# Performance work log

Hardware: AMD Instinct MI355X
Metric: run time of the kernel (lower is better)

Reference implementation:

```python
import jax, jax.numpy as jnp
import numpy as np

B, V, T, CIN, WEMB, H, NW = 32, 500, 24, 2, 4, 64, 8
C0 = CIN + WEMB  # 6 channels entering first layer


def _stglstm(x, supports, Wg, bg, Wo, bo, out_len=None, final_layer=False):
    # x: (B, C, V, T); supports: (S, V, V)
    Bb, C, Vv, Tt = x.shape
    T_steps = out_len if out_len is not None else Tt
    if final_layer:
        xs = jnp.broadcast_to(x[:, :, :, -1][None], (T_steps, Bb, C, Vv))
    else:
        xs = jnp.moveaxis(x, 3, 0)  # (T, B, C, V)

    def step(carry, xt):
        hx, cx = carry
        comb = xt + hx  # (B, C, V)
        feats = [comb]
        for s in range(supports.shape[0]):  # fixed small support_len loop
            x1 = jnp.einsum('bcv,vw->bcw', comb, supports[s])
            x2 = jnp.einsum('bcv,vw->bcw', x1, supports[s])
            feats += [x1, x2]  # order-2 diffusion
        g = jnp.concatenate(feats, axis=1)  # (B, 7C, V)
        gates = jnp.einsum('bgv,og->bov', g, Wg) + bg[None, :, None]  # (B, 4C, V)
        i, f, cg, o = jnp.split(gates, 4, axis=1)
        cy = jax.nn.sigmoid(f) * cx + jax.nn.sigmoid(i) * cg  # cellgate is linear (no tanh), as in source
        hy = jax.nn.sigmoid(o) * jnp.tanh(cy)
        return (hy, cy), hy

    h0 = jnp.zeros((Bb, C, Vv), x.dtype)
    _, hs = jax.lax.scan(step, (h0, h0), xs)  # hs: (T, B, C, V)
    hs = jnp.moveaxis(hs, 0, 3)  # (B, C, V, T)
    return jnp.einsum('bcvt,oc->bovt', hs, Wo) + bo[None, :, None, None]


def _se(x, Wa, Wb):
    y = x.mean(axis=(2, 3))  # (B, C) global avg pool
    y = jax.nn.sigmoid(jax.nn.relu(y @ Wa.T) @ Wb.T)
    return x * y[:, :, None, None]


def setup_inputs():
    key = jax.random.key(0)
    ks = jax.random.split(key, 24)

    def n(k, shape, s=0.05):
        return jax.random.normal(k, shape, jnp.float32) * s

    A = jax.random.uniform(ks[0], (3, V, V), jnp.float32)
    A = A / A.sum(-1, keepdims=True)  # row-stochastic random-walk matrices
    return {
        'x': n(ks[1], (B, CIN, V, T), 1.0),
        'supports': A,
        'w_type': jax.random.randint(ks[2], (B, V, T), 0, NW, dtype=jnp.int32),
        'Wemb': n(ks[3], (NW, WEMB)),
        'Wg0': n(ks[4], (4 * C0, 7 * C0)), 'bg0': jnp.zeros((4 * C0,), jnp.float32),
        'Wo0': n(ks[5], (H, C0)), 'bo0': jnp.zeros((H,), jnp.float32),
        'Ws0a': n(ks[6], (H // 16, H)), 'Ws0b': n(ks[7], (H, H // 16)),
        'Wg1': n(ks[8], (4 * H, 7 * H)), 'bg1': jnp.zeros((4 * H,), jnp.float32),
        'Wo1': n(ks[9], (H, H)), 'bo1': jnp.zeros((H,), jnp.float32),
        'Ws1a': n(ks[10], (H // 16, H)), 'Ws1b': n(ks[11], (H, H // 16)),
        'Wg2': n(ks[12], (4 * H, 7 * H)), 'bg2': jnp.zeros((4 * H,), jnp.float32),
        'Wo2': n(ks[13], (H, H)), 'bo2': jnp.zeros((H,), jnp.float32),
        'Wg3': n(ks[14], (4 * H, 7 * H)), 'bg3': jnp.zeros((4 * H,), jnp.float32),
        'Wo3': n(ks[15], (2, H)), 'bo3': jnp.zeros((2,), jnp.float32),
    }


def reference(x, supports, w_type, Wemb, Wg0, bg0, Wo0, bo0, Ws0a, Ws0b,
              Wg1, bg1, Wo1, bo1, Ws1a, Ws1b, Wg2, bg2, Wo2, bo2,
              Wg3, bg3, Wo3, bo3):
    w_vec = Wemb[w_type]  # (B, V, T, wemb)
    w_vec = jnp.transpose(w_vec, (0, 3, 1, 2))  # (B, wemb, V, T)
    h = jnp.concatenate([x, w_vec], axis=1)  # (B, CIN+wemb, V, T)
    h = _stglstm(h, supports, Wg0, bg0, Wo0, bo0)
    h = _se(h, Ws0a, Ws0b)
    h = _stglstm(h, supports, Wg1, bg1, Wo1, bo1)
    h = _se(h, Ws1a, Ws1b)
    h = _stglstm(h, supports, Wg2, bg2, Wo2, bo2)
    out = _stglstm(h, supports, Wg3, bg3, Wo3, bo3, out_len=T, final_layer=True)
    return out  # (B, 2, V, out_len)
```

## Files before the change

### kernel.cpp

```cpp
#include <hip/hip_runtime.h>
#include <math.h>

#define NV 500
#define NB 32
#define NT 24
#define NH 64

typedef _Float16 f16;
typedef _Float16 f16x8 __attribute__((ext_vector_type(8)));
typedef _Float16 f16x4 __attribute__((ext_vector_type(4)));
typedef float    f32x4 __attribute__((ext_vector_type(4)));

__device__ __forceinline__ float sigm(float x){ return 1.f/(1.f+expf(-x)); }

__global__ void k_a2(const float* __restrict__ A, float* __restrict__ A2)
{
    int idx = blockIdx.x*256 + threadIdx.x;
    if (idx >= 3*500*500) return;
    int wv = idx % 500; int rest = idx/500; int r = rest % 500; int s = rest/500;
    const float* Ar = A + ((size_t)s*500 + r)*500;
    const float* Ac = A + (size_t)s*500*500 + wv;
    float a = 0.f;
    for (int u = 0; u < 500; u++) a += Ar[u]*Ac[(size_t)u*500];
    A2[idx] = a;
}

__global__ void k_acat(const float* __restrict__ A, const float* __restrict__ A2,
                       f16* __restrict__ AcatT)
{
    int idx = blockIdx.x*256 + threadIdx.x;
    if (idx >= 3072*512) return;
    int k = idx & 511;
    int n = idx >> 9;
    int j = n >> 9, wv = n & 511;
    float val = 0.f;
    if (k < 500 && wv < 500) {
        int s = j >> 1;
        const float* M = (j & 1) ? A2 : A;
        val = M[((size_t)s*500 + k)*500 + wv];
    }
    AcatT[idx] = (f16)val;
}

__global__ void k_f2h(const float* __restrict__ src, f16* __restrict__ dst, int n)
{
    int idx = blockIdx.x*256 + threadIdx.x;
    if (idx < n) dst[idx] = (f16)src[idx];
}

__global__ __launch_bounds__(256)
void k_diff(const f16* __restrict__ Acv, const f16* __restrict__ Bt,
            f16* __restrict__ fout, int Mtot, int C, int G)
{
    __shared__ f16 lA[128*32];
    __shared__ f16 lB[128*32];
    const int tid = threadIdx.x;
    const int n0 = blockIdx.x*128, m0 = blockIdx.y*128;
    const int r0 = tid>>2, c0 = tid&3;
    const int swz0 = r0*32 + ((c0 ^ ((r0>>1)&3))<<3);
    const int swz1 = swz0 + 64*32;
    int mA0 = m0 + r0;      if (mA0 > Mtot-1) mA0 = Mtot-1;
    int mA1 = m0 + r0 + 64; if (mA1 > Mtot-1) mA1 = Mtot-1;
    const f16* gA0 = Acv + (size_t)mA0*512 + c0*8;
    const f16* gA1 = Acv + (size_t)mA1*512 + c0*8;
    const f16* gB0 = Bt + (size_t)(n0+r0)*512 + c0*8;
    const f16* gB1 = Bt + (size_t)(n0+r0+64)*512 + c0*8;

    const int w = tid>>6, lane = tid&63;
    const int wr = (w>>1)<<6, wc = (w&1)<<6;
    const int fm = lane&15, fk = lane>>4;
    const int fch = (fk ^ ((fm>>1)&3))<<3;

    f32x4 acc[4][4];
    #pragma unroll
    for (int i=0;i<4;i++)
        #pragma unroll
        for (int j=0;j<4;j++) acc[i][j] = (f32x4){0.f,0.f,0.f,0.f};

    f32x4 ra0 = *(const f32x4*)gA0, ra1 = *(const f32x4*)gA1;
    f32x4 rb0 = *(const f32x4*)gB0, rb1 = *(const f32x4*)gB1;

    for (int ks = 0; ks < 16; ks++) {
        __syncthreads();
        *(f32x4*)(lA + swz0) = ra0;  *(f32x4*)(lA + swz1) = ra1;
        *(f32x4*)(lB + swz0) = rb0;  *(f32x4*)(lB + swz1) = rb1;
        if (ks < 15) {
            int o = (ks+1)*32;
            ra0 = *(const f32x4*)(gA0 + o); ra1 = *(const f32x4*)(gA1 + o);
            rb0 = *(const f32x4*)(gB0 + o); rb1 = *(const f32x4*)(gB1 + o);
        }
        __syncthreads();
        f16x8 af[4], bf[4];
        #pragma unroll
        for (int i=0;i<4;i++) af[i] = *(const f16x8*)(lA + (wr + i*16 + fm)*32 + fch);
        #pragma unroll
        for (int j=0;j<4;j++) bf[j] = *(const f16x8*)(lB + (wc + j*16 + fm)*32 + fch);
        #pragma unroll
        for (int i=0;i<4;i++)
            #pragma unroll
            for (int j=0;j<4;j++)
                acc[i][j] = __builtin_amdgcn_mfma_f32_16x16x32_f16(af[i], bf[j], acc[i][j], 0, 0, 0);
    }

    #pragma unroll
    for (int j=0;j<4;j++) {
        int col = n0 + wc + j*16 + fm;
        int jb = col >> 9, wv = col & 511;
        if (wv >= 500) continue;
        #pragma unroll
        for (int i=0;i<4;i++) {
            int mb = m0 + wr + i*16 + fk*4;
            if (C == 64) {
                if (mb >= Mtot) continue;
                int b = mb >> 6, c = mb & 63;
                f16x4 h4;
                h4[0]=(f16)acc[i][j][0]; h4[1]=(f16)acc[i][j][1];
                h4[2]=(f16)acc[i][j][2]; h4[3]=(f16)acc[i][j][3];
                *(f16x4*)(fout + ((size_t)b*512 + wv)*G + C + jb*C + c) = h4;
            } else {
                #pragma unroll
                for (int r=0;r<4;r++) {
                    int m = mb + r;
                    if (m < Mtot) {
                        int b = m / C, c = m - b*C;
                        fout[((size_t)b*512 + wv)*G + C + jb*C + c] = (f16)acc[i][j][r];
                    }
                }
            }
        }
    }
}

__global__ __launch_bounds__(256)
void k_gates(const f16* __restrict__ fT, const f16* __restrict__ Wg,
             const float* __restrict__ bg, float* __restrict__ gT)
{
    __shared__ f16 lA[128*32];
    __shared__ f16 lB[128*32];
    const int tid = threadIdx.x;
    const int n0 = blockIdx.x*128, m0 = blockIdx.y*128, b = blockIdx.z;
    const f16* Ab = fT + (size_t)b*512*448;
    const int r0 = tid>>2, c0 = tid&3;
    const int swz0 = r0*32 + ((c0 ^ ((r0>>1)&3))<<3);
    const int swz1 = swz0 + 64*32;
    const f16* gA0 = Ab + (size_t)(m0+r0)*448 + c0*8;
    const f16* gA1 = Ab + (size_t)(m0+r0+64)*448 + c0*8;
    const f16* gB0 = Wg + (size_t)(n0+r0)*448 + c0*8;
    const f16* gB1 = Wg + (size_t)(n0+r0+64)*448 + c0*8;

    const int w = tid>>6, lane = tid&63;
    const int wr = (w>>1)<<6, wc = (w&1)<<6;
    const int fm = lane&15, fk = lane>>4;
    const int fch = (fk ^ ((fm>>1)&3))<<3;

    f32x4 acc[4][4];
    #pragma unroll
    for (int i=0;i<4;i++)
        #pragma unroll
        for (int j=0;j<4;j++) acc[i][j] = (f32x4){0.f,0.f,0.f,0.f};

    f32x4 ra0 = *(const f32x4*)gA0, ra1 = *(const f32x4*)gA1;
    f32x4 rb0 = *(const f32x4*)gB0, rb1 = *(const f32x4*)gB1;

    for (int ks = 0; ks < 14; ks++) {
        __syncthreads();
        *(f32x4*)(lA + swz0) = ra0;  *(f32x4*)(lA + swz1) = ra1;
        *(f32x4*)(lB + swz0) = rb0;  *(f32x4*)(lB + swz1) = rb1;
        if (ks < 13) {
            int o = (ks+1)*32;
            ra0 = *(const f32x4*)(gA0 + o); ra1 = *(const f32x4*)(gA1 + o);
            rb0 = *(const f32x4*)(gB0 + o); rb1 = *(const f32x4*)(gB1 + o);
        }
        __syncthreads();
        f16x8 af[4], bf[4];
        #pragma unroll
        for (int i=0;i<4;i++) af[i] = *(const f16x8*)(lA + (wr + i*16 + fm)*32 + fch);
        #pragma unroll
        for (int j=0;j<4;j++) bf[j] = *(const f16x8*)(lB + (wc + j*16 + fm)*32 + fch);
        #pragma unroll
        for (int i=0;i<4;i++)
            #pragma unroll
            for (int j=0;j<4;j++)
                acc[i][j] = __builtin_amdgcn_mfma_f32_16x16x32_f16(af[i], bf[j], acc[i][j], 0, 0, 0);
    }

    #pragma unroll
    for (int j=0;j<4;j++) {
        int o = n0 + wc + j*16 + fm;
        float bias = bg[o];
        #pragma unroll
        for (int i=0;i<4;i++) {
            int vb = m0 + wr + i*16 + fk*4;
            #pragma unroll
            for (int r=0;r<4;r++) {
                int v = vb + r;
                if (v < 500)
                    gT[((size_t)b*512 + v)*256 + o] = acc[i][j][r] + bias;
            }
        }
    }
}

__global__ __launch_bounds__(256)
void k_comb(const void* __restrict__ src, int srcF16, int Cin,
            const float* __restrict__ Wo, const float* __restrict__ bo,
            const float* __restrict__ se, const f16* __restrict__ hprev,
            f16* __restrict__ fT, f16* __restrict__ ccv)
{
    __shared__ float WoS[64*64];
    __shared__ float seS[64], boS[64];
    __shared__ f16 combS[64*72];
    int b = blockIdx.y, v0 = blockIdx.x*64;
    int tid = threadIdx.x;
    if (Cin > 0) {
        for (int i = tid; i < 64*Cin; i += 256) WoS[i] = Wo[i];
        if (tid < 64) { boS[tid] = bo[tid]; seS[tid] = se ? se[b*64+tid] : 1.f; }
    }
    __syncthreads();
    int vloc = tid>>2, part = tid&3;
    int v = v0 + vloc;
    float val[16];
    if (Cin == 0) {
        const float* x3 = (const float*)src + ((size_t)b*512 + v)*64 + part*16;
        #pragma unroll
        for (int k=0;k<16;k++) val[k] = x3[k];
    } else {
        float acc[16];
        #pragma unroll
        for (int k=0;k<16;k++) acc[k] = 0.f;
        if (srcF16) {
            const f16* sp = (const f16*)src + ((size_t)b*512 + v)*64;
            for (int cc=0; cc<Cin; cc++) {
                float xv = (float)sp[cc];
                #pragma unroll
                for (int k=0;k<16;k++) acc[k] += WoS[(part*16+k)*Cin + cc]*xv;
            }
        } else {
            const float* sp = (const float*)src + ((size_t)b*512 + v)*(size_t)Cin;
            for (int cc=0; cc<Cin; cc++) {
                float xv = sp[cc];
                #pragma unroll
                for (int k=0;k<16;k++) acc[k] += WoS[(part*16+k)*Cin + cc]*xv;
            }
        }
        #pragma unroll
        for (int k=0;k<16;k++) { int c = part*16+k; val[k] = seS[c]*(acc[k] + boS[c]); }
    }
    if (hprev) {
        const f16* hp = hprev + ((size_t)b*512 + v)*64 + part*16;
        #pragma unroll
        for (int k=0;k<16;k++) val[k] += (float)hp[k];
    }
    if (v >= 500) {
        #pragma unroll
        for (int k=0;k<16;k++) val[k] = 0.f;
    }
    #pragma unroll
    for (int k=0;k<16;k++) combS[vloc*72 + part*16 + k] = (f16)val[k];
    __syncthreads();
    {
        int vl = tid>>2, p = tid&3;
        f32x4 d0 = *(f32x4*)(combS + vl*72 + p*16);
        f32x4 d1 = *(f32x4*)(combS + vl*72 + p*16 + 8);
        f16* dst = fT + ((size_t)b*512 + (v0+vl))*448 + p*16;
        *(f32x4*)dst = d0; *(f32x4*)(dst+8) = d1;
    }
    {
        int c = tid>>2, p = tid&3;
        alignas(16) f16 tmp[16];
        #pragma unroll
        for (int k=0;k<16;k++) tmp[k] = combS[(p*16+k)*72 + c];
        f16* dst = ccv + ((size_t)b*64 + c)*512 + v0 + p*16;
        *(f32x4*)dst = *(f32x4*)tmp; *(f32x4*)(dst+8) = *(f32x4*)(tmp+8);
    }
}

__global__ void k_lstm(const float* __restrict__ gT, float* __restrict__ cst,
                       f16* __restrict__ hdst, int first)
{
    int id = blockIdx.x*4 + (threadIdx.x>>6);
    if (id >= NB*500) return;
    int b = id / 500, v = id - b*500;
    int c = threadIdx.x & 63;
    const float* g = gT + ((size_t)b*512 + v)*256;
    float gi = g[c], gf = g[64+c], gc = g[128+c], go = g[192+c];
    size_t ci = ((size_t)b*512 + v)*64 + c;
    float cx = first ? 0.f : cst[ci];
    float cy = sigm(gf)*cx + sigm(gi)*gc;
    cst[ci] = cy;
    hdst[ci] = (f16)(sigm(go)*tanhf(cy));
}

__global__ void k_lstm3out(const float* __restrict__ gT, float* __restrict__ cst,
                           f16* __restrict__ hdst, const float* __restrict__ Wo3,
                           const float* __restrict__ bo3, float* __restrict__ out,
                           int t, int first)
{
    int id = blockIdx.x*4 + (threadIdx.x>>6);
    if (id >= NB*500) return;
    int b = id / 500, v = id - b*500;
    int c = threadIdx.x & 63;
    const float* g = gT + ((size_t)b*512 + v)*256;
    float gi = g[c], gf = g[64+c], gc = g[128+c], go = g[192+c];
    size_t ci = ((size_t)b*512 + v)*64 + c;
    float cx = first ? 0.f : cst[ci];
    float cy = sigm(gf)*cx + sigm(gi)*gc;
    cst[ci] = cy;
    float hy = sigm(go)*tanhf(cy);
    hdst[ci] = (f16)hy;
    float r0 = Wo3[c]*hy, r1 = Wo3[64+c]*hy;
    #pragma unroll
    for (int s = 32; s > 0; s >>= 1) {
        r0 += __shfl_down(r0, s, 64);
        r1 += __shfl_down(r1, s, 64);
    }
    if (c == 0) {
        out[((size_t)(b*2+0)*500 + v)*24 + t] = r0 + bo3[0];
        out[((size_t)(b*2+1)*500 + v)*24 + t] = r1 + bo3[1];
    }
}

__global__ void k_comb0(const float* __restrict__ x, const int* __restrict__ wt,
                        const float* __restrict__ Wemb, const float* __restrict__ hs0T,
                        f16* __restrict__ f0T, f16* __restrict__ ccv0, int t)
{
    int b = blockIdx.y;
    int v = blockIdx.x*256 + threadIdx.x;
    if (v >= 512) return;
    if (v >= 500) {
        #pragma unroll
        for (int c=0;c<6;c++) ccv0[((size_t)b*6 + c)*512 + v] = (f16)0.f;
        return;
    }
    float vals[6];
    vals[0] = x[((size_t)(b*2+0)*500 + v)*24 + t];
    vals[1] = x[((size_t)(b*2+1)*500 + v)*24 + t];
    int wty = wt[((size_t)b*500 + v)*24 + t];
    vals[2] = Wemb[wty*4+0]; vals[3] = Wemb[wty*4+1];
    vals[4] = Wemb[wty*4+2]; vals[5] = Wemb[wty*4+3];
    if (t > 0) {
        const float* hp = hs0T + (((size_t)(t-1)*NB + b)*512 + v)*6;
        #pragma unroll
        for (int c=0;c<6;c++) vals[c] += hp[c];
    }
    #pragma unroll
    for (int c=0;c<6;c++) {
        f16 h = (f16)vals[c];
        f0T[((size_t)b*512 + v)*42 + c] = h;
        ccv0[((size_t)b*6 + c)*512 + v] = h;
    }
}

__global__ void k_gates0(const float* __restrict__ Wg, const float* __restrict__ bgv,
                         const f16* __restrict__ f0T, float* __restrict__ g0T)
{
    __shared__ float WgS[24*42];
    for (int i = threadIdx.x; i < 24*42; i += 256) WgS[i] = Wg[i];
    __syncthreads();
    int idx = blockIdx.x*256 + threadIdx.x;
    if (idx >= NB*24*500) return;
    int v = idx % 500; int rest = idx/500; int o = rest % 24; int b = rest/24;
    const f16* fp = f0T + ((size_t)b*512 + v)*42;
    float a = bgv[o];
    #pragma unroll
    for (int g = 0; g < 42; g++) a += WgS[o*42+g]*(float)fp[g];
    g0T[((size_t)b*512 + v)*24 + o] = a;
}

__global__ void k_lstm0(const float* __restrict__ g0T, float* __restrict__ cst0,
                        float* __restrict__ hs0T, int t)
{
    int idx = blockIdx.x*256 + threadIdx.x;
    if (idx >= NB*500*6) return;
    int c = idx % 6; int rest = idx/6; int v = rest % 500; int b = rest/500;
    const float* g = g0T + ((size_t)b*512 + v)*24;
    float gi = g[c], gf = g[6+c], gc = g[12+c], go = g[18+c];
    size_t ci = ((size_t)b*500 + v)*6 + c;
    float cx = t ? cst0[ci] : 0.f;
    float cy = sigm(gf)*cx + sigm(gi)*gc;
    cst0[ci] = cy;
    hs0T[(((size_t)t*NB + b)*512 + v)*6 + c] = sigm(go)*tanhf(cy);
}

__global__ void k_mean0(const float* __restrict__ hs0T, float* __restrict__ mean0)
{
    int b = blockIdx.x;
    float acc[6] = {0,0,0,0,0,0};
    for (int i = threadIdx.x; i < 24*500; i += 256) {
        int tt = i/500, v = i - tt*500;
        const float* p = hs0T + (((size_t)tt*NB + b)*512 + v)*6;
        #pragma unroll
        for (int c=0;c<6;c++) acc[c] += p[c];
    }
    __shared__ float red[256];
    for (int c=0;c<6;c++) {
        red[threadIdx.x] = acc[c]; __syncthreads();
        for (int s=128;s>0;s>>=1) { if (threadIdx.x<s) red[threadIdx.x]+=red[threadIdx.x+s]; __syncthreads(); }
        if (threadIdx.x==0) mean0[b*6+c] = red[0]/12000.f;
        __syncthreads();
    }
}

__global__ void k_mean1(const f16* __restrict__ hs1T, float* __restrict__ mean1)
{
    int cg = blockIdx.x, b = blockIdx.y;
    float acc[8] = {0,0,0,0,0,0,0,0};
    for (int i = threadIdx.x; i < 24*500; i += 256) {
        int tt = i/500, v = i - tt*500;
        const f16* p = hs1T + (((size_t)tt*NB + b)*512 + v)*64 + cg*8;
        #pragma unroll
        for (int c=0;c<8;c++) acc[c] += (float)p[c];
    }
    __shared__ float red[256];
    for (int c=0;c<8;c++) {
        red[threadIdx.x] = acc[c]; __syncthreads();
        for (int s=128;s>0;s>>=1) { if (threadIdx.x<s) red[threadIdx.x]+=red[threadIdx.x+s]; __syncthreads(); }
        if (threadIdx.x==0) mean1[b*64 + cg*8 + c] = red[0]/12000.f;
        __syncthreads();
    }
}

__global__ void k_se(const float* __restrict__ meanhs, const float* __restrict__ Wo,
                     const float* __restrict__ bo, int Cin,
                     const float* __restrict__ Wa, const float* __restrict__ Wb,
                     float* __restrict__ se)
{
    int b = blockIdx.x; int c = threadIdx.x;
    __shared__ float y[64]; __shared__ float a[4];
    float acc = bo[c];
    for (int j = 0; j < Cin; j++) acc += Wo[(size_t)c*Cin + j] * meanhs[b*Cin + j];
    y[c] = acc;
    __syncthreads();
    if (c < 4) {
        float s = 0.f;
        for (int j = 0; j < 64; j++) s += Wa[c*64 + j] * y[j];
        a[c] = fmaxf(s, 0.f);
    }
    __syncthreads();
    float s = 0.f;
    #pragma unroll
    for (int j = 0; j < 4; j++) s += Wb[c*4 + j] * a[j];
    se[b*64 + c] = 1.f/(1.f + expf(-s));
}

__global__ void k_x3(const f16* __restrict__ h, const float* __restrict__ Wo,
                     const float* __restrict__ bo, float* __restrict__ x3T)
{
    int idx = blockIdx.x*256 + threadIdx.x;
    if (idx >= NB*500*64) return;
    int c = idx & 63; int rest = idx >> 6; int v = rest % 500; int b = rest/500;
    const f16* hp = h + ((size_t)b*512 + v)*64;
    float a = bo[c];
    #pragma unroll 8
    for (int cc = 0; cc < 64; cc++) a += Wo[c*64 + cc]*(float)hp[cc];
    x3T[((size_t)b*512 + v)*64 + c] = a;
}

extern "C" void kernel_launch(void* const* d_in, const int* in_sizes, int n_in,
                              void* d_out, int out_size, void* d_ws, size_t ws_size,
                              hipStream_t stream)
{
    const float* x    = (const float*)d_in[0];
    const float* sup  = (const float*)d_in[1];
    const int*   wt   = (const int*)  d_in[2];
    const float* Wemb = (const float*)d_in[3];
    const float* Wg0  = (const float*)d_in[4];
    const float* bg0  = (const float*)d_in[5];
    const float* Wo0  = (const float*)d_in[6];
    const float* bo0  = (const float*)d_in[7];
    const float* Wa0  = (const float*)d_in[8];
    const float* Wb0  = (const float*)d_in[9];
    const float* Wg1  = (const float*)d_in[10];
    const float* bg1  = (const float*)d_in[11];
    const float* Wo1  = (const float*)d_in[12];
    const float* bo1  = (const float*)d_in[13];
    const float* Wa1  = (const float*)d_in[14];
    const float* Wb1  = (const float*)d_in[15];
    const float* Wg2  = (const float*)d_in[16];
    const float* bg2  = (const float*)d_in[17];
    const float* Wo2  = (const float*)d_in[18];
    const float* bo2  = (const float*)d_in[19];
    const float* Wg3  = (const float*)d_in[20];
    const float* bg3  = (const float*)d_in[21];
    const float* Wo3  = (const float*)d_in[22];
    const float* bo3  = (const float*)d_in[23];
    float* out = (float*)d_out;
    (void)in_sizes; (void)n_in; (void)out_size; (void)ws_size;

    char* ws = (char*)d_ws;
    size_t off = 0;
    f16*   AcatT  = (f16*)(ws + off);   off += (size_t)3072*512*2;
    float* A2     = (float*)(ws + off); off += (size_t)3*500*500*4;
    f16*   WgF1   = (f16*)(ws + off);   off += (size_t)256*448*2;
    f16*   WgF2   = (f16*)(ws + off);   off += (size_t)256*448*2;
    f16*   WgF3   = (f16*)(ws + off);   off += (size_t)256*448*2;
    f16*   comb_cv= (f16*)(ws + off);   off += (size_t)2048*512*2;
    f16*   ccv0   = (f16*)(ws + off);   off += (size_t)192*512*2;
    f16*   featsT = (f16*)(ws + off);   off += (size_t)NB*512*448*2;
    f16*   f0T    = (f16*)(ws + off);   off += (size_t)NB*512*42*2;
    float* gatesT = (float*)(ws + off); off += (size_t)NB*512*256*4;
    float* g0T    = (float*)(ws + off); off += (size_t)NB*512*24*4;
    float* hs0T   = (float*)(ws + off); off += (size_t)NT*NB*512*6*4;
    f16*   hs1T   = (f16*)(ws + off);   off += (size_t)NT*NB*512*64*2;
    f16*   hT     = (f16*)(ws + off);   off += (size_t)NB*512*64*2;
    float* cstT   = (float*)(ws + off); off += (size_t)NB*512*64*4;
    float* cst0   = (float*)(ws + off); off += (size_t)NB*500*6*4;
    float* x3T    = (float*)(ws + off); off += (size_t)NB*512*64*4;
    float* mean0  = (float*)(ws + off); off += 8192;
    float* se0    = (float*)(ws + off); off += 8192;
    float* mean1  = (float*)(ws + off); off += 8192;
    float* se1    = (float*)(ws + off); off += 8192;

    const size_t sliceH = (size_t)NB*512*64;
    const size_t slice0 = (size_t)NB*512*6;

    k_a2  <<<(3*500*500 + 255)/256, 256, 0, stream>>>(sup, A2);
    k_acat<<<(3072*512 + 255)/256, 256, 0, stream>>>(sup, A2, AcatT);
    k_f2h <<<(256*448 + 255)/256, 256, 0, stream>>>(Wg1, WgF1, 256*448);
    k_f2h <<<(256*448 + 255)/256, 256, 0, stream>>>(Wg2, WgF2, 256*448);
    k_f2h <<<(256*448 + 255)/256, 256, 0, stream>>>(Wg3, WgF3, 256*448);

    for (int t = 0; t < NT; t++) {
        k_comb0 <<<dim3(2, NB), 256, 0, stream>>>(x, wt, Wemb, hs0T, f0T, ccv0, t);
        k_diff  <<<dim3(24, 2), 256, 0, stream>>>(ccv0, AcatT, f0T, 192, 6, 42);
        k_gates0<<<(NB*24*500 + 255)/256, 256, 0, stream>>>(Wg0, bg0, f0T, g0T);
        k_lstm0 <<<(NB*500*6 + 255)/256, 256, 0, stream>>>(g0T, cst0, hs0T, t);
    }
    k_mean0<<<NB, 256, 0, stream>>>(hs0T, mean0);
    k_se   <<<NB, 64, 0, stream>>>(mean0, Wo0, bo0, 6, Wa0, Wb0, se0);

    for (int t = 0; t < NT; t++) {
        k_comb <<<dim3(8, NB), 256, 0, stream>>>(hs0T + (size_t)t*slice0, 0, 6,
                 Wo0, bo0, se0, t ? hs1T + (size_t)(t-1)*sliceH : (const f16*)nullptr,
                 featsT, comb_cv);
        k_diff <<<dim3(24, 16), 256, 0, stream>>>(comb_cv, AcatT, featsT, 2048, 64, 448);
        k_gates<<<dim3(2, 4, NB), 256, 0, stream>>>(featsT, WgF1, bg1, gatesT);
        k_lstm <<<4000, 256, 0, stream>>>(gatesT, cstT, hs1T + (size_t)t*sliceH, t == 0);
    }
    k_mean1<<<dim3(8, NB), 256, 0, stream>>>(hs1T, mean1);
    k_se   <<<NB, 64, 0, stream>>>(mean1, Wo1, bo1, 64, Wa1, Wb1, se1);

    for (int t = 0; t < NT; t++) {
        k_comb <<<dim3(8, NB), 256, 0, stream>>>(hs1T + (size_t)t*sliceH, 1, 64,
                 Wo1, bo1, se1, t ? hT : (const f16*)nullptr, featsT, comb_cv);
        k_diff <<<dim3(24, 16), 256, 0, stream>>>(comb_cv, AcatT, featsT, 2048, 64, 448);
        k_gates<<<dim3(2, 4, NB), 256, 0, stream>>>(featsT, WgF2, bg2, gatesT);
        k_lstm <<<4000, 256, 0, stream>>>(gatesT, cstT, hT, t == 0);
    }
    k_x3<<<(NB*500*64 + 255)/256, 256, 0, stream>>>(hT, Wo2, bo2, x3T);

    for (int t = 0; t < NT; t++) {
        k_comb <<<dim3(8, NB), 256, 0, stream>>>(x3T, 0, 0,
                 (const float*)nullptr, (const float*)nullptr, (const float*)nullptr,
                 t ? hT : (const f16*)nullptr, featsT, comb_cv);
        k_diff <<<dim3(24, 16), 256, 0, stream>>>(comb_cv, AcatT, featsT, 2048, 64, 448);
        k_gates<<<dim3(2, 4, NB), 256, 0, stream>>>(featsT, WgF3, bg3, gatesT);
        k_lstm3out<<<4000, 256, 0, stream>>>(gatesT, cstT, hT, Wo3, bo3, out, t, t == 0);
    }
}
```

Measured before the change: 4.362 ms.

## Fuse LSTM update with next-step comb, hoist input projections, async LDS GEMM loads

Merges the per-step LSTM cell update with building the next step's combined input and its transposed copy, removing one launch and one round trip of hidden state per timestep. The per-layer input projections (Wo, bias and SE scale) are precomputed for all timesteps in one batched kernel rather than inside each step, and layer 0's gates GEMV is fused with its LSTM update. The GEMM kernels switch to global_load_lds direct-to-LDS loads with double-buffered LDS, so each k-step needs one barrier instead of two. The trade-offs are a larger workspace for the precomputed projections and a bigger LDS footprint per block.

```diff
diff --git a/kernel.cpp b/kernel.cpp
--- a/kernel.cpp
+++ b/kernel.cpp
@@ -12,6 +12,13 @@
 typedef float    f32x4 __attribute__((ext_vector_type(4)));
 
 __device__ __forceinline__ float sigm(float x){ return 1.f/(1.f+expf(-x)); }
+
+__device__ __forceinline__ void gld16(const f16* g, f16* l)
+{
+    __builtin_amdgcn_global_load_lds(
+        (const __attribute__((address_space(1))) void*)g,
+        (__attribute__((address_space(3))) void*)l, 16, 0, 0);
+}
 
 __global__ void k_a2(const float* __restrict__ A, float* __restrict__ A2)
 {
@@ -52,24 +59,26 @@
 void k_diff(const f16* __restrict__ Acv, const f16* __restrict__ Bt,
             f16* __restrict__ fout, int Mtot, int C, int G)
 {
-    __shared__ f16 lA[128*32];
-    __shared__ f16 lB[128*32];
+    __shared__ f16 lds[4*4096];
     const int tid = threadIdx.x;
     const int n0 = blockIdx.x*128, m0 = blockIdx.y*128;
-    const int r0 = tid>>2, c0 = tid&3;
-    const int swz0 = r0*32 + ((c0 ^ ((r0>>1)&3))<<3);
-    const int swz1 = swz0 + 64*32;
-    int mA0 = m0 + r0;      if (mA0 > Mtot-1) mA0 = Mtot-1;
-    int mA1 = m0 + r0 + 64; if (mA1 > Mtot-1) mA1 = Mtot-1;
-    const f16* gA0 = Acv + (size_t)mA0*512 + c0*8;
-    const f16* gA1 = Acv + (size_t)mA1*512 + c0*8;
-    const f16* gB0 = Bt + (size_t)(n0+r0)*512 + c0*8;
-    const f16* gB1 = Bt + (size_t)(n0+r0+64)*512 + c0*8;
-
     const int w = tid>>6, lane = tid&63;
-    const int wr = (w>>1)<<6, wc = (w&1)<<6;
+
+    const int ra = w*16 + (lane>>2);
+    const int rb = ra + 64;
+    const int ca = ((lane&3) ^ ((ra>>1)&3))<<3;
+    const int cb = ((lane&3) ^ ((rb>>1)&3))<<3;
+    int mA0 = m0 + ra; if (mA0 > Mtot-1) mA0 = Mtot-1;
+    int mA1 = m0 + rb; if (mA1 > Mtot-1) mA1 = Mtot-1;
+    const f16* gA0 = Acv + (size_t)mA0*512 + ca;
+    const f16* gA1 = Acv + (size_t)mA1*512 + cb;
+    const f16* gB0 = Bt + (size_t)(n0+ra)*512 + ca;
+    const f16* gB1 = Bt + (size_t)(n0+rb)*512 + cb;
+    const int lwb = w*512;
+
     const int fm = lane&15, fk = lane>>4;
     const int fch = (fk ^ ((fm>>1)&3))<<3;
+    const int wr = (w>>1)<<6, wc = (w&1)<<6;
 
     f32x4 acc[4][4];
     #pragma unroll
@@ -77,29 +86,36 @@
         #pragma unroll
         for (int j=0;j<4;j++) acc[i][j] = (f32x4){0.f,0.f,0.f,0.f};
 
-    f32x4 ra0 = *(const f32x4*)gA0, ra1 = *(const f32x4*)gA1;
-    f32x4 rb0 = *(const f32x4*)gB0, rb1 = *(const f32x4*)gB1;
-
+    gld16(gA0, lds + lwb);
+    gld16(gA1, lds + 2048 + lwb);
+    gld16(gB0, lds + 4096 + lwb);
+    gld16(gB1, lds + 6144 + lwb);
+    __syncthreads();
+
+    #pragma unroll 2
     for (int ks = 0; ks < 16; ks++) {
-        __syncthreads();
-        *(f32x4*)(lA + swz0) = ra0;  *(f32x4*)(lA + swz1) = ra1;
-        *(f32x4*)(lB + swz0) = rb0;  *(f32x4*)(lB + swz1) = rb1;
+        const int cur = ks & 1;
         if (ks < 15) {
-            int o = (ks+1)*32;
-            ra0 = *(const f32x4*)(gA0 + o); ra1 = *(const f32x4*)(gA1 + o);
-            rb0 = *(const f32x4*)(gB0 + o); rb1 = *(const f32x4*)(gB1 + o);
-        }
-        __syncthreads();
+            f16* Ln = lds + (cur^1)*8192;
+            const int o = (ks+1)*32;
+            gld16(gA0 + o, Ln + lwb);
+            gld16(gA1 + o, Ln + 2048 + lwb);
+            gld16(gB0 + o, Ln + 4096 + lwb);
+            gld16(gB1 + o, Ln + 6144 + lwb);
+        }
+        const f16* La = lds + cur*8192;
+        const f16* Lb = La + 4096;
         f16x8 af[4], bf[4];
         #pragma unroll
-        for (int i=0;i<4;i++) af[i] = *(const f16x8*)(lA + (wr + i*16 + fm)*32 + fch);
-        #pragma unroll
-        for (int j=0;j<4;j++) bf[j] = *(const f16x8*)(lB + (wc + j*16 + fm)*32 + fch);
+        for (int i=0;i<4;i++) af[i] = *(const f16x8*)(La + (wr + i*16 + fm)*32 + fch);
+        #pragma unroll
+        for (int j=0;j<4;j++) bf[j] = *(const f16x8*)(Lb + (wc + j*16 + fm)*32 + fch);
         #pragma unroll
         for (int i=0;i<4;i++)
             #pragma unroll
             for (int j=0;j<4;j++)
                 acc[i][j] = __builtin_amdgcn_mfma_f32_16x16x32_f16(af[i], bf[j], acc[i][j], 0, 0, 0);
+        __syncthreads();
     }
 
     #pragma unroll
@@ -135,23 +151,25 @@
 void k_gates(const f16* __restrict__ fT, const f16* __restrict__ Wg,
              const float* __restrict__ bg, float* __restrict__ gT)
 {
-    __shared__ f16 lA[128*32];
-    __shared__ f16 lB[128*32];
+    __shared__ f16 lds[4*4096];
     const int tid = threadIdx.x;
     const int n0 = blockIdx.x*128, m0 = blockIdx.y*128, b = blockIdx.z;
     const f16* Ab = fT + (size_t)b*512*448;
-    const int r0 = tid>>2, c0 = tid&3;
-    const int swz0 = r0*32 + ((c0 ^ ((r0>>1)&3))<<3);
-    const int swz1 = swz0 + 64*32;
-    const f16* gA0 = Ab + (size_t)(m0+r0)*448 + c0*8;
-    const f16* gA1 = Ab + (size_t)(m0+r0+64)*448 + c0*8;
-    const f16* gB0 = Wg + (size_t)(n0+r0)*448 + c0*8;
-    const f16* gB1 = Wg + (size_t)(n0+r0+64)*448 + c0*8;
-
     const int w = tid>>6, lane = tid&63;
-    const int wr = (w>>1)<<6, wc = (w&1)<<6;
+
+    const int ra = w*16 + (lane>>2);
+    const int rb = ra + 64;
+    const int ca = ((lane&3) ^ ((ra>>1)&3))<<3;
+    const int cb = ((lane&3) ^ ((rb>>1)&3))<<3;
+    const f16* gA0 = Ab + (size_t)(m0+ra)*448 + ca;
+    const f16* gA1 = Ab + (size_t)(m0+rb)*448 + cb;
+    const f16* gB0 = Wg + (size_t)(n0+ra)*448 + ca;
+    const f16* gB1 = Wg + (size_t)(n0+rb)*448 + cb;
+    const int lwb = w*512;
+
     const int fm = lane&15, fk = lane>>4;
     const int fch = (fk ^ ((fm>>1)&3))<<3;
+    const int wr = (w>>1)<<6, wc = (w&1)<<6;
 
     f32x4 acc[4][4];
     #pragma unroll
@@ -159,29 +177,36 @@
         #pragma unroll
         for (int j=0;j<4;j++) acc[i][j] = (f32x4){0.f,0.f,0.f,0.f};
 
-    f32x4 ra0 = *(const f32x4*)gA0, ra1 = *(const f32x4*)gA1;
-    f32x4 rb0 = *(const f32x4*)gB0, rb1 = *(const f32x4*)gB1;
-
+    gld16(gA0, lds + lwb);
+    gld16(gA1, lds + 2048 + lwb);
+    gld16(gB0, lds + 4096 + lwb);
+    gld16(gB1, lds + 6144 + lwb);
+    __syncthreads();
+
+    #pragma unroll 2
     for (int ks = 0; ks < 14; ks++) {
-        __syncthreads();
-        *(f32x4*)(lA + swz0) = ra0;  *(f32x4*)(lA + swz1) = ra1;
-        *(f32x4*)(lB + swz0) = rb0;  *(f32x4*)(lB + swz1) = rb1;
+        const int cur = ks & 1;
         if (ks < 13) {
-            int o = (ks+1)*32;
-            ra0 = *(const f32x4*)(gA0 + o); ra1 = *(const f32x4*)(gA1 + o);
-            rb0 = *(const f32x4*)(gB0 + o); rb1 = *(const f32x4*)(gB1 + o);
-        }
-        __syncthreads();
+            f16* Ln = lds + (cur^1)*8192;
+            const int o = (ks+1)*32;
+            gld16(gA0 + o, Ln + lwb);
+            gld16(gA1 + o, Ln + 2048 + lwb);
+            gld16(gB0 + o, Ln + 4096 + lwb);
+            gld16(gB1 + o, Ln + 6144 + lwb);
+        }
+        const f16* La = lds + cur*8192;
+        const f16* Lb = La + 4096;
         f16x8 af[4], bf[4];
         #pragma unroll
-        for (int i=0;i<4;i++) af[i] = *(const f16x8*)(lA + (wr + i*16 + fm)*32 + fch);
-        #pragma unroll
-        for (int j=0;j<4;j++) bf[j] = *(const f16x8*)(lB + (wc + j*16 + fm)*32 + fch);
+        for (int i=0;i<4;i++) af[i] = *(const f16x8*)(La + (wr + i*16 + fm)*32 + fch);
+        #pragma unroll
+        for (int j=0;j<4;j++) bf[j] = *(const f16x8*)(Lb + (wc + j*16 + fm)*32 + fch);
         #pragma unroll
         for (int i=0;i<4;i++)
             #pragma unroll
             for (int j=0;j<4;j++)
                 acc[i][j] = __builtin_amdgcn_mfma_f32_16x16x32_f16(af[i], bf[j], acc[i][j], 0, 0, 0);
+        __syncthreads();
     }
 
     #pragma unroll
@@ -202,184 +227,242 @@
 }
 
 __global__ __launch_bounds__(256)
-void k_comb(const void* __restrict__ src, int srcF16, int Cin,
-            const float* __restrict__ Wo, const float* __restrict__ bo,
-            const float* __restrict__ se, const f16* __restrict__ hprev,
-            f16* __restrict__ fT, f16* __restrict__ ccv)
+void k_lstmcomb(const float* __restrict__ gT, float* __restrict__ cst,
+                const f16* __restrict__ Xn, f16* __restrict__ hsave,
+                const float* __restrict__ Wo3, const float* __restrict__ bo3,
+                float* __restrict__ out, int t,
+                f16* __restrict__ fT, f16* __restrict__ ccv,
+                int first, int writecomb)
+{
+    __shared__ f16 combS[64*68];
+    const int b = blockIdx.y, v0 = blockIdx.x*64;
+    const int tid = threadIdx.x, vl = tid>>2, p = tid&3;
+    const int v = v0 + vl;
+    const size_t row = (size_t)b*512 + v;
+    const float* g = gT + row*256 + p*16;
+    f32x4 g4[4][4];
+    #pragma unroll
+    for (int q = 0; q < 4; q++)
+        #pragma unroll
+        for (int k4 = 0; k4 < 4; k4++)
+            g4[q][k4] = *(const f32x4*)(g + q*64 + k4*4);
+
+    float* cp = cst + row*64 + p*16;
+    float hy[16];
+    #pragma unroll
+    for (int k4 = 0; k4 < 4; k4++) {
+        f32x4 cx4 = first ? (f32x4){0.f,0.f,0.f,0.f} : *(const f32x4*)(cp + k4*4);
+        f32x4 cy4;
+        #pragma unroll
+        for (int e = 0; e < 4; e++) {
+            float gi = g4[0][k4][e], gf = g4[1][k4][e], gc = g4[2][k4][e], go = g4[3][k4][e];
+            float cy = sigm(gf)*cx4[e] + sigm(gi)*gc;
+            cy4[e] = cy;
+            hy[k4*4+e] = sigm(go)*tanhf(cy);
+        }
+        *(f32x4*)(cp + k4*4) = cy4;
+    }
+
+    if (hsave) {
+        alignas(16) f16 tmp[16];
+        #pragma unroll
+        for (int k=0;k<16;k++) tmp[k] = (f16)hy[k];
+        f16* hp = hsave + row*64 + p*16;
+        *(f32x4*)hp = *(f32x4*)tmp;
+        *(f32x4*)(hp+8) = *(f32x4*)(tmp+8);
+    }
+
+    if (out) {
+        float r0 = 0.f, r1 = 0.f;
+        #pragma unroll
+        for (int k=0;k<16;k++){ r0 += Wo3[p*16+k]*hy[k]; r1 += Wo3[64+p*16+k]*hy[k]; }
+        r0 += __shfl_xor(r0, 1, 64); r0 += __shfl_xor(r0, 2, 64);
+        r1 += __shfl_xor(r1, 1, 64); r1 += __shfl_xor(r1, 2, 64);
+        if (p == 0 && v < 500) {
+            out[((size_t)(b*2+0)*500 + v)*24 + t] = r0 + bo3[0];
+            out[((size_t)(b*2+1)*500 + v)*24 + t] = r1 + bo3[1];
+        }
+    }
+
+    if (writecomb) {
+        alignas(16) f16 c16[16];
+        if (v < 500) {
+            const f16* xp = Xn + row*64 + p*16;
+            alignas(16) f16 xv[16];
+            *(f32x4*)xv = *(const f32x4*)xp;
+            *(f32x4*)(xv+8) = *(const f32x4*)(xp+8);
+            #pragma unroll
+            for (int k=0;k<16;k++) c16[k] = (f16)((float)xv[k] + hy[k]);
+        } else {
+            #pragma unroll
+            for (int k=0;k<16;k++) c16[k] = (f16)0.f;
+        }
+        f16* fp = fT + row*448 + p*16;
+        *(f32x4*)fp = *(f32x4*)c16;
+        *(f32x4*)(fp+8) = *(f32x4*)(c16+8);
+        #pragma unroll
+        for (int k=0;k<16;k++) combS[vl*68 + p*16 + k] = c16[k];
+        __syncthreads();
+        const int c = tid>>2, j = tid&3;
+        alignas(16) f16 tmp[16];
+        #pragma unroll
+        for (int k=0;k<16;k++) tmp[k] = combS[(j*16+k)*68 + c];
+        f16* dst = ccv + ((size_t)b*64 + c)*512 + v0 + j*16;
+        *(f32x4*)dst = *(f32x4*)tmp;
+        *(f32x4*)(dst+8) = *(f32x4*)(tmp+8);
+    }
+}
+
+__global__ __launch_bounds__(256)
+void k_seed(const f16* __restrict__ X0, f16* __restrict__ fT, f16* __restrict__ ccv)
+{
+    __shared__ f16 combS[64*68];
+    const int b = blockIdx.y, v0 = blockIdx.x*64;
+    const int tid = threadIdx.x, vl = tid>>2, p = tid&3;
+    const int v = v0 + vl;
+    const size_t row = (size_t)b*512 + v;
+    alignas(16) f16 c16[16];
+    if (v < 500) {
+        const f16* xp = X0 + row*64 + p*16;
+        *(f32x4*)c16 = *(const f32x4*)xp;
+        *(f32x4*)(c16+8) = *(const f32x4*)(xp+8);
+    } else {
+        #pragma unroll
+        for (int k=0;k<16;k++) c16[k] = (f16)0.f;
+    }
+    f16* fp = fT + row*448 + p*16;
+    *(f32x4*)fp = *(f32x4*)c16;
+    *(f32x4*)(fp+8) = *(f32x4*)(c16+8);
+    #pragma unroll
+    for (int k=0;k<16;k++) combS[vl*68 + p*16 + k] = c16[k];
+    __syncthreads();
+    const int c = tid>>2, j = tid&3;
+    alignas(16) f16 tmp[16];
+    #pragma unroll
+    for (int k=0;k<16;k++) tmp[k] = combS[(j*16+k)*68 + c];
+    f16* dst = ccv + ((size_t)b*64 + c)*512 + v0 + j*16;
+    *(f32x4*)dst = *(f32x4*)tmp;
+    *(f32x4*)(dst+8) = *(f32x4*)(tmp+8);
+}
+
+__global__ __launch_bounds__(256)
+void k_xproj(const void* __restrict__ src, int srcF16, int Cin,
+             const float* __restrict__ Wo, const float* __restrict__ bo,
+             const float* __restrict__ se, f16* __restrict__ X)
 {
     __shared__ float WoS[64*64];
-    __shared__ float seS[64], boS[64];
-    __shared__ f16 combS[64*72];
-    int b = blockIdx.y, v0 = blockIdx.x*64;
+    __shared__ float boS[64], seS[64];
+    const int b = blockIdx.y, t = blockIdx.z, v0 = blockIdx.x*64;
+    const int tid = threadIdx.x;
+    for (int i = tid; i < 64*Cin; i += 256) WoS[i] = Wo[i];
+    if (tid < 64) { boS[tid] = bo[tid]; seS[tid] = se ? se[b*64+tid] : 1.f; }
+    __syncthreads();
+    const int vl = tid>>2, p = tid&3;
+    const int v = v0 + vl;
+    const size_t row = ((size_t)t*NB + b)*512 + v;
+    float acc[16];
+    #pragma unroll
+    for (int k=0;k<16;k++) acc[k] = 0.f;
+    if (srcF16) {
+        const f16* sp = (const f16*)src + row*Cin;
+        for (int cc = 0; cc < Cin; cc++) {
+            float xv = (float)sp[cc];
+            #pragma unroll
+            for (int k=0;k<16;k++) acc[k] += WoS[(p*16+k)*Cin + cc]*xv;
+        }
+    } else {
+        const float* sp = (const float*)src + row*Cin;
+        for (int cc = 0; cc < Cin; cc++) {
+            float xv = sp[cc];
+            #pragma unroll
+            for (int k=0;k<16;k++) acc[k] += WoS[(p*16+k)*Cin + cc]*xv;
+        }
+    }
+    alignas(16) f16 o16[16];
+    #pragma unroll
+    for (int k=0;k<16;k++) { int c = p*16+k; o16[k] = (f16)(seS[c]*(acc[k] + boS[c])); }
+    f16* xp = X + row*64 + p*16;
+    *(f32x4*)xp = *(f32x4*)o16;
+    *(f32x4*)(xp+8) = *(f32x4*)(o16+8);
+}
+
+__global__ void k_xe(const float* __restrict__ x, const int* __restrict__ wt,
+                     const float* __restrict__ Wemb, float* __restrict__ XE)
+{
+    int id = blockIdx.x*256 + threadIdx.x;
+    if (id >= NT*NB*512) return;
+    int v = id & 511; int r = id >> 9; int b = r & 31; int t = r >> 5;
+    float vals[6] = {0.f,0.f,0.f,0.f,0.f,0.f};
+    if (v < 500) {
+        vals[0] = x[((size_t)(b*2+0)*500 + v)*24 + t];
+        vals[1] = x[((size_t)(b*2+1)*500 + v)*24 + t];
+        int wty = wt[((size_t)b*500 + v)*24 + t];
+        vals[2] = Wemb[wty*4+0]; vals[3] = Wemb[wty*4+1];
+        vals[4] = Wemb[wty*4+2]; vals[5] = Wemb[wty*4+3];
+    }
+    float* xe = XE + (size_t)id*6;
+    #pragma unroll
+    for (int c = 0; c < 6; c++) xe[c] = vals[c];
+}
+
+__global__ void k_seed0(const float* __restrict__ XE, f16* __restrict__ f0T,
+                        f16* __restrict__ ccv0)
+{
+    int id = blockIdx.x*256 + threadIdx.x;
+    if (id >= NB*512) return;
+    int v = id & 511, b = id >> 9;
+    const float* xe = XE + (size_t)id*6;
+    #pragma unroll
+    for (int c = 0; c < 6; c++) {
+        f16 h = (v < 500) ? (f16)xe[c] : (f16)0.f;
+        f0T[(size_t)id*42 + c] = h;
+        ccv0[((size_t)b*6 + c)*512 + v] = h;
+    }
+}
+
+__global__ __launch_bounds__(256)
+void k_glstm0(f16* f0T, const float* __restrict__ Wg0,
+              const float* __restrict__ bg0, float* __restrict__ cst0,
+              float* __restrict__ hs0T, const float* __restrict__ XE,
+              f16* __restrict__ ccv0, int t)
+{
+    __shared__ float WgS[24*42];
+    __shared__ float bgS[24];
     int tid = threadIdx.x;
-    if (Cin > 0) {
-        for (int i = tid; i < 64*Cin; i += 256) WoS[i] = Wo[i];
-        if (tid < 64) { boS[tid] = bo[tid]; seS[tid] = se ? se[b*64+tid] : 1.f; }
-    }
+    for (int i = tid; i < 24*42; i += 256) WgS[i] = Wg0[i];
+    if (tid < 24) bgS[tid] = bg0[tid];
     __syncthreads();
-    int vloc = tid>>2, part = tid&3;
-    int v = v0 + vloc;
-    float val[16];
-    if (Cin == 0) {
-        const float* x3 = (const float*)src + ((size_t)b*512 + v)*64 + part*16;
-        #pragma unroll
-        for (int k=0;k<16;k++) val[k] = x3[k];
-    } else {
-        float acc[16];
-        #pragma unroll
-        for (int k=0;k<16;k++) acc[k] = 0.f;
-        if (srcF16) {
-            const f16* sp = (const f16*)src + ((size_t)b*512 + v)*64;
-            for (int cc=0; cc<Cin; cc++) {
-                float xv = (float)sp[cc];
-                #pragma unroll
-                for (int k=0;k<16;k++) acc[k] += WoS[(part*16+k)*Cin + cc]*xv;
-            }
-        } else {
-            const float* sp = (const float*)src + ((size_t)b*512 + v)*(size_t)Cin;
-            for (int cc=0; cc<Cin; cc++) {
-                float xv = sp[cc];
-                #pragma unroll
-                for (int k=0;k<16;k++) acc[k] += WoS[(part*16+k)*Cin + cc]*xv;
-            }
-        }
-        #pragma unroll
-        for (int k=0;k<16;k++) { int c = part*16+k; val[k] = seS[c]*(acc[k] + boS[c]); }
-    }
-    if (hprev) {
-        const f16* hp = hprev + ((size_t)b*512 + v)*64 + part*16;
-        #pragma unroll
-        for (int k=0;k<16;k++) val[k] += (float)hp[k];
-    }
-    if (v >= 500) {
-        #pragma unroll
-        for (int k=0;k<16;k++) val[k] = 0.f;
-    }
-    #pragma unroll
-    for (int k=0;k<16;k++) combS[vloc*72 + part*16 + k] = (f16)val[k];
-    __syncthreads();
-    {
-        int vl = tid>>2, p = tid&3;
-        f32x4 d0 = *(f32x4*)(combS + vl*72 + p*16);
-        f32x4 d1 = *(f32x4*)(combS + vl*72 + p*16 + 8);
-        f16* dst = fT + ((size_t)b*512 + (v0+vl))*448 + p*16;
-        *(f32x4*)dst = d0; *(f32x4*)(dst+8) = d1;
-    }
-    {
-        int c = tid>>2, p = tid&3;
-        alignas(16) f16 tmp[16];
-        #pragma unroll
-        for (int k=0;k<16;k++) tmp[k] = combS[(p*16+k)*72 + c];
-        f16* dst = ccv + ((size_t)b*64 + c)*512 + v0 + p*16;
-        *(f32x4*)dst = *(f32x4*)tmp; *(f32x4*)(dst+8) = *(f32x4*)(tmp+8);
-    }
-}
-
-__global__ void k_lstm(const float* __restrict__ gT, float* __restrict__ cst,
-                       f16* __restrict__ hdst, int first)
-{
-    int id = blockIdx.x*4 + (threadIdx.x>>6);
+    int id = blockIdx.x*256 + tid;
     if (id >= NB*500) return;
     int b = id / 500, v = id - b*500;
-    int c = threadIdx.x & 63;
-    const float* g = gT + ((size_t)b*512 + v)*256;
-    float gi = g[c], gf = g[64+c], gc = g[128+c], go = g[192+c];
-    size_t ci = ((size_t)b*512 + v)*64 + c;
-    float cx = first ? 0.f : cst[ci];
-    float cy = sigm(gf)*cx + sigm(gi)*gc;
-    cst[ci] = cy;
-    hdst[ci] = (f16)(sigm(go)*tanhf(cy));
-}
-
-__global__ void k_lstm3out(const float* __restrict__ gT, float* __restrict__ cst,
-                           f16* __restrict__ hdst, const float* __restrict__ Wo3,
-                           const float* __restrict__ bo3, float* __restrict__ out,
-                           int t, int first)
-{
-    int id = blockIdx.x*4 + (threadIdx.x>>6);
-    if (id >= NB*500) return;
-    int b = id / 500, v = id - b*500;
-    int c = threadIdx.x & 63;
-    const float* g = gT + ((size_t)b*512 + v)*256;
-    float gi = g[c], gf = g[64+c], gc = g[128+c], go = g[192+c];
-    size_t ci = ((size_t)b*512 + v)*64 + c;
-    float cx = first ? 0.f : cst[ci];
-    float cy = sigm(gf)*cx + sigm(gi)*gc;
-    cst[ci] = cy;
-    float hy = sigm(go)*tanhf(cy);
-    hdst[ci] = (f16)hy;
-    float r0 = Wo3[c]*hy, r1 = Wo3[64+c]*hy;
-    #pragma unroll
-    for (int s = 32; s > 0; s >>= 1) {
-        r0 += __shfl_down(r0, s, 64);
-        r1 += __shfl_down(r1, s, 64);
-    }
-    if (c == 0) {
-        out[((size_t)(b*2+0)*500 + v)*24 + t] = r0 + bo3[0];
-        out[((size_t)(b*2+1)*500 + v)*24 + t] = r1 + bo3[1];
-    }
-}
-
-__global__ void k_comb0(const float* __restrict__ x, const int* __restrict__ wt,
-                        const float* __restrict__ Wemb, const float* __restrict__ hs0T,
-                        f16* __restrict__ f0T, f16* __restrict__ ccv0, int t)
-{
-    int b = blockIdx.y;
-    int v = blockIdx.x*256 + threadIdx.x;
-    if (v >= 512) return;
-    if (v >= 500) {
-        #pragma unroll
-        for (int c=0;c<6;c++) ccv0[((size_t)b*6 + c)*512 + v] = (f16)0.f;
-        return;
-    }
-    float vals[6];
-    vals[0] = x[((size_t)(b*2+0)*500 + v)*24 + t];
-    vals[1] = x[((size_t)(b*2+1)*500 + v)*24 + t];
-    int wty = wt[((size_t)b*500 + v)*24 + t];
-    vals[2] = Wemb[wty*4+0]; vals[3] = Wemb[wty*4+1];
-    vals[4] = Wemb[wty*4+2]; vals[5] = Wemb[wty*4+3];
-    if (t > 0) {
-        const float* hp = hs0T + (((size_t)(t-1)*NB + b)*512 + v)*6;
-        #pragma unroll
-        for (int c=0;c<6;c++) vals[c] += hp[c];
-    }
-    #pragma unroll
-    for (int c=0;c<6;c++) {
-        f16 h = (f16)vals[c];
-        f0T[((size_t)b*512 + v)*42 + c] = h;
-        ccv0[((size_t)b*6 + c)*512 + v] = h;
-    }
-}
-
-__global__ void k_gates0(const float* __restrict__ Wg, const float* __restrict__ bgv,
-                         const f16* __restrict__ f0T, float* __restrict__ g0T)
-{
-    __shared__ float WgS[24*42];
-    for (int i = threadIdx.x; i < 24*42; i += 256) WgS[i] = Wg[i];
-    __syncthreads();
-    int idx = blockIdx.x*256 + threadIdx.x;
-    if (idx >= NB*24*500) return;
-    int v = idx % 500; int rest = idx/500; int o = rest % 24; int b = rest/24;
     const f16* fp = f0T + ((size_t)b*512 + v)*42;
-    float a = bgv[o];
-    #pragma unroll
-    for (int g = 0; g < 42; g++) a += WgS[o*42+g]*(float)fp[g];
-    g0T[((size_t)b*512 + v)*24 + o] = a;
-}
-
-__global__ void k_lstm0(const float* __restrict__ g0T, float* __restrict__ cst0,
-                        float* __restrict__ hs0T, int t)
-{
-    int idx = blockIdx.x*256 + threadIdx.x;
-    if (idx >= NB*500*6) return;
-    int c = idx % 6; int rest = idx/6; int v = rest % 500; int b = rest/500;
-    const float* g = g0T + ((size_t)b*512 + v)*24;
-    float gi = g[c], gf = g[6+c], gc = g[12+c], go = g[18+c];
-    size_t ci = ((size_t)b*500 + v)*6 + c;
-    float cx = t ? cst0[ci] : 0.f;
-    float cy = sigm(gf)*cx + sigm(gi)*gc;
-    cst0[ci] = cy;
-    hs0T[(((size_t)t*NB + b)*512 + v)*6 + c] = sigm(go)*tanhf(cy);
+    float fv[42];
+    #pragma unroll
+    for (int g = 0; g < 42; g++) fv[g] = (float)fp[g];
+    float gates[24];
+    #pragma unroll
+    for (int o = 0; o < 24; o++) {
+        float a = bgS[o];
+        #pragma unroll
+        for (int g = 0; g < 42; g++) a += WgS[o*42+g]*fv[g];
+        gates[o] = a;
+    }
+    size_t hrow = (((size_t)t*NB + b)*512 + v)*6;
+    const float* xe = XE + (((size_t)(t+1)*NB + b)*512 + v)*6;
+    #pragma unroll
+    for (int c = 0; c < 6; c++) {
+        size_t ci = ((size_t)b*500 + v)*6 + c;
+        float cx = t ? cst0[ci] : 0.f;
+        float cy = sigm(gates[6+c])*cx + sigm(gates[c])*gates[12+c];
+        cst0[ci] = cy;
+        float h = sigm(gates[18+c])*tanhf(cy);
+        hs0T[hrow + c] = h;
+        if (t < 23) {
+            float cmb = xe[c] + h;
+            f0T[((size_t)b*512 + v)*42 + c] = (f16)cmb;
+            ccv0[((size_t)b*6 + c)*512 + v] = (f16)cmb;
+        }
+    }
 }
 
 __global__ void k_mean0(const float* __restrict__ hs0T, float* __restrict__ mean0)
@@ -441,19 +524,6 @@
     #pragma unroll
     for (int j = 0; j < 4; j++) s += Wb[c*4 + j] * a[j];
     se[b*64 + c] = 1.f/(1.f + expf(-s));
-}
-
-__global__ void k_x3(const f16* __restrict__ h, const float* __restrict__ Wo,
-                     const float* __restrict__ bo, float* __restrict__ x3T)
-{
-    int idx = blockIdx.x*256 + threadIdx.x;
-    if (idx >= NB*500*64) return;
-    int c = idx & 63; int rest = idx >> 6; int v = rest % 500; int b = rest/500;
-    const f16* hp = h + ((size_t)b*512 + v)*64;
-    float a = bo[c];
-    #pragma unroll 8
-    for (int cc = 0; cc < 64; cc++) a += Wo[c*64 + cc]*(float)hp[cc];
-    x3T[((size_t)b*512 + v)*64 + c] = a;
 }
 
 extern "C" void kernel_launch(void* const* d_in, const int* in_sizes, int n_in,
@@ -499,62 +569,68 @@
     f16*   featsT = (f16*)(ws + off);   off += (size_t)NB*512*448*2;
     f16*   f0T    = (f16*)(ws + off);   off += (size_t)NB*512*42*2;
     float* gatesT = (float*)(ws + off); off += (size_t)NB*512*256*4;
-    float* g0T    = (float*)(ws + off); off += (size_t)NB*512*24*4;
     float* hs0T   = (float*)(ws + off); off += (size_t)NT*NB*512*6*4;
     f16*   hs1T   = (f16*)(ws + off);   off += (size_t)NT*NB*512*64*2;
     f16*   hT     = (f16*)(ws + off);   off += (size_t)NB*512*64*2;
     float* cstT   = (float*)(ws + off); off += (size_t)NB*512*64*4;
     float* cst0   = (float*)(ws + off); off += (size_t)NB*500*6*4;
-    float* x3T    = (float*)(ws + off); off += (size_t)NB*512*64*4;
+    f16*   Xbuf   = (f16*)(ws + off);   off += (size_t)NT*NB*512*64*2;
+    f16*   X3     = (f16*)(ws + off);   off += (size_t)NB*512*64*2;
     float* mean0  = (float*)(ws + off); off += 8192;
     float* se0    = (float*)(ws + off); off += 8192;
     float* mean1  = (float*)(ws + off); off += 8192;
     float* se1    = (float*)(ws + off); off += 8192;
 
+    float* XE = gatesT;
+
     const size_t sliceH = (size_t)NB*512*64;
-    const size_t slice0 = (size_t)NB*512*6;
 
     k_a2  <<<(3*500*500 + 255)/256, 256, 0, stream>>>(sup, A2);
     k_acat<<<(3072*512 + 255)/256, 256, 0, stream>>>(sup, A2, AcatT);
     k_f2h <<<(256*448 + 255)/256, 256, 0, stream>>>(Wg1, WgF1, 256*448);
     k_f2h <<<(256*448 + 255)/256, 256, 0, stream>>>(Wg2, WgF2, 256*448);
     k_f2h <<<(256*448 + 255)/256, 256, 0, stream>>>(Wg3, WgF3, 256*448);
-
+    k_xe  <<<(NT*NB*512)/256, 256, 0, stream>>>(x, wt, Wemb, XE);
+
+    k_seed0<<<(NB*512)/256, 256, 0, stream>>>(XE, f0T, ccv0);
     for (int t = 0; t < NT; t++) {
-        k_comb0 <<<dim3(2, NB), 256, 0, stream>>>(x, wt, Wemb, hs0T, f0T, ccv0, t);
         k_diff  <<<dim3(24, 2), 256, 0, stream>>>(ccv0, AcatT, f0T, 192, 6, 42);
-        k_gates0<<<(NB*24*500 + 255)/256, 256, 0, stream>>>(Wg0, bg0, f0T, g0T);
-        k_lstm0 <<<(NB*500*6 + 255)/256, 256, 0, stream>>>(g0T, cst0, hs0T, t);
+        k_glstm0<<<(NB*500 + 255)/256, 256, 0, stream>>>(f0T, Wg0, bg0, cst0, hs0T, XE, ccv0, t);
     }
     k_mean0<<<NB, 256, 0, stream>>>(hs0T, mean0);
     k_se   <<<NB, 64, 0, stream>>>(mean0, Wo0, bo0, 6, Wa0, Wb0, se0);
 
+    k_xproj<<<dim3(8, NB, NT), 256, 0, stream>>>(hs0T, 0, 6, Wo0, bo0, se0, Xbuf);
+    k_seed <<<dim3(8, NB), 256, 0, stream>>>(Xbuf, featsT, comb_cv);
     for (int t = 0; t < NT; t++) {
-        k_comb <<<dim3(8, NB), 256, 0, stream>>>(hs0T + (size_t)t*slice0, 0, 6,
-                 Wo0, bo0, se0, t ? hs1T + (size_t)(t-1)*sliceH : (const f16*)nullptr,
-                 featsT, comb_cv);
         k_diff <<<dim3(24, 16), 256, 0, stream>>>(comb_cv, AcatT, featsT, 2048, 64, 448);
         k_gates<<<dim3(2, 4, NB), 256, 0, stream>>>(featsT, WgF1, bg1, gatesT);
-        k_lstm <<<4000, 256, 0, stream>>>(gatesT, cstT, hs1T + (size_t)t*sliceH, t == 0);
+        k_lstmcomb<<<dim3(8, NB), 256, 0, stream>>>(gatesT, cstT,
+                 (t < 23) ? Xbuf + (size_t)(t+1)*sliceH : (const f16*)nullptr,
+                 hs1T + (size_t)t*sliceH, nullptr, nullptr, nullptr, t,
+                 featsT, comb_cv, t == 0, t < 23);
     }
     k_mean1<<<dim3(8, NB), 256, 0, stream>>>(hs1T, mean1);
     k_se   <<<NB, 64, 0, stream>>>(mean1, Wo1, bo1, 64, Wa1, Wb1, se1);
 
+    k_xproj<<<dim3(8, NB, NT), 256, 0, stream>>>(hs1T, 1, 64, Wo1, bo1, se1, Xbuf);
+    k_seed <<<dim3(8, NB), 256, 0, stream>>>(Xbuf, featsT, comb_cv);
     for (int t = 0; t < NT; t++) {
-        k_comb <<<dim3(8, NB), 256, 0, stream>>>(hs1T + (size_t)t*sliceH, 1, 64,
-                 Wo1, bo1, se1, t ? hT : (const f16*)nullptr, featsT, comb_cv);
         k_diff <<<dim3(24, 16), 256, 0, stream>>>(comb_cv, AcatT, featsT, 2048, 64, 448);
         k_gates<<<dim3(2, 4, NB), 256, 0, stream>>>(featsT, WgF2, bg2, gatesT);
-        k_lstm <<<4000, 256, 0, stream>>>(gatesT, cstT, hT, t == 0);
-    }
-    k_x3<<<(NB*500*64 + 255)/256, 256, 0, stream>>>(hT, Wo2, bo2, x3T);
-
+        k_lstmcomb<<<dim3(8, NB), 256, 0, stream>>>(gatesT, cstT,
+                 (t < 23) ? Xbuf + (size_t)(t+1)*sliceH : (const f16*)nullptr,
+                 hT, nullptr, nullptr, nullptr, t,
+                 featsT, comb_cv, t == 0, t < 23);
+    }
+
+    k_xproj<<<dim3(8, NB, 1), 256, 0, stream>>>(hT, 1, 64, Wo2, bo2, nullptr, X3);
+    k_seed <<<dim3(8, NB), 256, 0, stream>>>(X3, featsT, comb_cv);
     for (int t = 0; t < NT; t++) {
-        k_comb <<<dim3(8, NB), 256, 0, stream>>>(x3T, 0, 0,
-                 (const float*)nullptr, (const float*)nullptr, (const float*)nullptr,
-                 t ? hT : (const f16*)nullptr, featsT, comb_cv);
         k_diff <<<dim3(24, 16), 256, 0, stream>>>(comb_cv, AcatT, featsT, 2048, 64, 448);
         k_gates<<<dim3(2, 4, NB), 256, 0, stream>>>(featsT, WgF3, bg3, gatesT);
-        k_lstm3out<<<4000, 256, 0, stream>>>(gatesT, cstT, hT, Wo3, bo3, out, t, t == 0);
-    }
-}
+        k_lstmcomb<<<dim3(8, NB), 256, 0, stream>>>(gatesT, cstT, X3,
+                 nullptr, Wo3, bo3, out, t,
+                 featsT, comb_cv, t == 0, t < 23);
+    }
+}
```

After: 5.771 ms. +32.3%, slower.
